# Kernel tuning notes

Hardware: AMD Instinct MI355X
Metric: run time of the kernel (lower is better)

Reference implementation:

```python
import jax, jax.numpy as jnp
import numpy as np

N = 100000
M = 1600000
IN_C = 64
OUT_C = 64


def setup_inputs() -> dict:
    key = jax.random.key(0)
    k1, k2, k3 = jax.random.split(key, 3)
    x = jax.random.normal(k1, (N, IN_C), dtype=jnp.float32)
    edge_index = jax.random.randint(k2, (2, M), 0, N, dtype=jnp.int64)
    # glorot-initialized linear weight (no bias in lin)
    limit = np.sqrt(6.0 / (IN_C + OUT_C))
    W = jax.random.uniform(k3, (IN_C, OUT_C), dtype=jnp.float32, minval=-limit, maxval=limit)
    b = jnp.zeros((OUT_C,), dtype=jnp.float32)  # zeros() init for bias
    return {"x": x, "edge_index": edge_index, "W": W, "b": b}


def reference(x, edge_index, W, b):
    # x: [N, in_c] -> lin -> [N, out_c]
    h = x @ W
    n = x.shape[0]
    row, col = edge_index[0], edge_index[1]  # source, target

    # add self loops (fill_value = 1.0 since improved=False)
    loop = jnp.arange(n, dtype=edge_index.dtype)
    row = jnp.concatenate([row, loop])
    col = jnp.concatenate([col, loop])
    w = jnp.ones(row.shape[0], dtype=h.dtype)  # edge_weight defaults to ones

    # symmetric gcn normalization: deg over target nodes
    deg = jax.ops.segment_sum(w, col, num_segments=n)
    deg_inv_sqrt = deg ** -0.5
    deg_inv_sqrt = jnp.where(jnp.isinf(deg_inv_sqrt), 0.0, deg_inv_sqrt)
    norm = deg_inv_sqrt[row] * w * deg_inv_sqrt[col]  # [M+N]

    # spmm: aggregate normalized source messages at targets
    msgs = norm[:, None] * h[row]  # [M+N, out_c]
    out = jax.ops.segment_sum(msgs, col, num_segments=n)  # [N, out_c]
    return out + b
```

## Files before the change

kernel.cpp:

```cpp
#include <hip/hip_runtime.h>

#define N_NODES 100000
#define M_EDGES 1600000
#define CH 64
#define NPB 256
#define NB ((N_NODES + NPB - 1) / NPB)
#define PART_CHUNK 8192
#define PART_BLOCKS ((M_EDGES + PART_CHUNK - 1) / PART_CHUNK)
#define REG_E 12
#define GROWS 192
#define GBLKS ((N_NODES + GROWS - 1) / GROWS)

__device__ __forceinline__ unsigned int pack_bf16x2(float a, float b) {
    unsigned int ua = __float_as_uint(a);
    ua = (ua + 0x7fffu + ((ua >> 16) & 1u)) >> 16;
    unsigned int ub = __float_as_uint(b);
    ub = (ub + 0x7fffu + ((ub >> 16) & 1u)) >> 16;
    return ua | (ub << 16);
}
__device__ __forceinline__ float bf_lo(unsigned int u) { return __uint_as_float(u << 16); }
__device__ __forceinline__ float bf_hi(unsigned int u) { return __uint_as_float(u & 0xffff0000u); }

__global__ __launch_bounds__(256) void k_bhist(const int* __restrict__ col, int* __restrict__ T) {
    __shared__ int h[NB];
    int tid = threadIdx.x;
    for (int i = tid; i < NB; i += 256) h[i] = 0;
    __syncthreads();
    int start = blockIdx.x * PART_CHUNK;
    int end = min(M_EDGES, start + PART_CHUNK);
    for (int e = start + tid; e < end; e += 256) atomicAdd(&h[col[e] >> 8], 1);
    __syncthreads();
    for (int i = tid; i < NB; i += 256) T[blockIdx.x * NB + i] = h[i];
}

__global__ __launch_bounds__(256) void k_colsum(int* __restrict__ T, int* __restrict__ tot) {
    __shared__ int s[256];
    int b = blockIdx.x, t = threadIdx.x;
    int v = (t < PART_BLOCKS) ? T[t * NB + b] : 0;
    s[t] = v;
    __syncthreads();
    for (int off = 1; off < 256; off <<= 1) {
        int tv = (t >= off) ? s[t - off] : 0;
        __syncthreads();
        s[t] += tv;
        __syncthreads();
    }
    if (t < PART_BLOCKS) T[t * NB + b] = s[t] - v;
    if (t == 255) tot[b] = s[255];
}

__global__ __launch_bounds__(512) void k_bucket_scan(const int* __restrict__ tot, int* __restrict__ bbase) {
    __shared__ int s[512];
    int v = (threadIdx.x < NB) ? tot[threadIdx.x] : 0;
    s[threadIdx.x] = v;
    __syncthreads();
    for (int off = 1; off < 512; off <<= 1) {
        int t = (threadIdx.x >= off) ? s[threadIdx.x - off] : 0;
        __syncthreads();
        s[threadIdx.x] += t;
        __syncthreads();
    }
    if (threadIdx.x < NB) bbase[threadIdx.x] = s[threadIdx.x] - v;
    if (threadIdx.x == NB - 1) bbase[NB] = s[NB - 1];
}

__global__ __launch_bounds__(256) void k_partition(const int* __restrict__ row, const int* __restrict__ col,
                                                   const int* __restrict__ bbase, const int* __restrict__ T,
                                                   unsigned int* __restrict__ pairs) {
    __shared__ int h[NB];
    int tid = threadIdx.x;
    int c = blockIdx.x;
    for (int i = tid; i < NB; i += 256) h[i] = bbase[i] + T[c * NB + i];
    __syncthreads();
    int start = c * PART_CHUNK;
    int end = min(M_EDGES, start + PART_CHUNK);
    for (int e = start + tid; e < end; e += 256) {
        int cc = col[e];
        int pos = atomicAdd(&h[cc >> 8], 1);
        pairs[pos] = ((unsigned int)row[e] << 8) | (unsigned int)(cc & 255);
    }
}

__global__ __launch_bounds__(512) void k_fine(const int* __restrict__ bbase,
                                              unsigned int* __restrict__ pairs, int* __restrict__ node_start,
                                              float* __restrict__ dis) {
    __shared__ int lcnt[NPB];
    __shared__ int lcur[NPB];
    __shared__ int ss[NPB];
    int b = blockIdx.x, t = threadIdx.x;
    int s0 = bbase[b], e0 = bbase[b + 1];

    if (t < NPB) lcnt[t] = 0;
    __syncthreads();

    unsigned int reg[REG_E];
#pragma unroll
    for (int k = 0; k < REG_E; k++) {
        int e = s0 + t + k * 512;
        if (e < e0) {
            unsigned int p = pairs[e];
            reg[k] = p;
            atomicAdd(&lcnt[p & 255u], 1);
        }
    }
    __syncthreads();

    int v = 0;
    if (t < NPB) { v = lcnt[t]; ss[t] = v; }
    __syncthreads();
    for (int off = 1; off < NPB; off <<= 1) {
        int tv = (t < NPB && t >= off) ? ss[t - off] : 0;
        __syncthreads();
        if (t < NPB) ss[t] += tv;
        __syncthreads();
    }
    if (t < NPB) {
        int excl = ss[t] - v;
        lcur[t] = excl;
        int node = b * NPB + t;
        if (node < N_NODES) {
            node_start[node] = s0 + excl;
            dis[node] = 1.0f / sqrtf((float)(v + 1));
        }
        if (b == NB - 1 && t == 0) node_start[N_NODES] = e0;
    }
    __syncthreads();

#pragma unroll
    for (int k = 0; k < REG_E; k++) {
        int e = s0 + t + k * 512;
        if (e < e0) {
            unsigned int p = reg[k];
            int pos = atomicAdd(&lcur[p & 255u], 1);
            pairs[s0 + pos] = p >> 8;
        }
    }
}

__global__ __launch_bounds__(256) void k_gemm_g(const float* __restrict__ x, const float* __restrict__ W,
                                                const float* __restrict__ dis, unsigned int* __restrict__ g2) {
    __shared__ float sW[64][64];
    __shared__ float sXf[GROWS * 65];
    int t = threadIdx.x;
    int row0 = blockIdx.x * GROWS;
    int nrows = min(GROWS, N_NODES - row0);

    for (int i = t; i < 64 * 64; i += 256) sW[i >> 6][i & 63] = W[i];
    const float4* xv = (const float4*)x;
    for (int idx = t; idx < GROWS * 16; idx += 256) {
        int r = idx >> 4, c4 = idx & 15;
        float4 v = (r < nrows) ? xv[(size_t)(row0 + r) * 16 + c4] : make_float4(0.f, 0.f, 0.f, 0.f);
        sXf[r * 65 + c4 * 4 + 0] = v.x;
        sXf[r * 65 + c4 * 4 + 1] = v.y;
        sXf[r * 65 + c4 * 4 + 2] = v.z;
        sXf[r * 65 + c4 * 4 + 3] = v.w;
    }
    __syncthreads();

    int q = t >> 6;
    int rid = t & 63;
    int c0 = q * 16;
    float acc0[16], acc1[16], acc2[16];
#pragma unroll
    for (int j = 0; j < 16; j++) { acc0[j] = 0.f; acc1[j] = 0.f; acc2[j] = 0.f; }

    for (int k = 0; k < 64; k++) {
        float xv0 = sXf[rid * 65 + k];
        float xv1 = sXf[(rid + 64) * 65 + k];
        float xv2 = sXf[(rid + 128) * 65 + k];
        const float4* wp = (const float4*)&sW[k][c0];
        float4 w0 = wp[0], w1 = wp[1], w2 = wp[2], w3 = wp[3];
        float wv[16] = {w0.x, w0.y, w0.z, w0.w, w1.x, w1.y, w1.z, w1.w,
                        w2.x, w2.y, w2.z, w2.w, w3.x, w3.y, w3.z, w3.w};
#pragma unroll
        for (int j = 0; j < 16; j++) {
            acc0[j] += xv0 * wv[j];
            acc1[j] += xv1 * wv[j];
            acc2[j] += xv2 * wv[j];
        }
    }

#pragma unroll
    for (int jr = 0; jr < 3; jr++) {
        int r = rid + jr * 64;
        int gr = row0 + r;
        if (r < nrows) {
            float* accp = (jr == 0) ? acc0 : (jr == 1) ? acc1 : acc2;
            float d = dis[gr];
            uint4 wlo, whi;
            wlo.x = pack_bf16x2(d * accp[0], d * accp[1]);
            wlo.y = pack_bf16x2(d * accp[2], d * accp[3]);
            wlo.z = pack_bf16x2(d * accp[4], d * accp[5]);
            wlo.w = pack_bf16x2(d * accp[6], d * accp[7]);
            whi.x = pack_bf16x2(d * accp[8], d * accp[9]);
            whi.y = pack_bf16x2(d * accp[10], d * accp[11]);
            whi.z = pack_bf16x2(d * accp[12], d * accp[13]);
            whi.w = pack_bf16x2(d * accp[14], d * accp[15]);
            unsigned int base = (unsigned int)gr * 32 + q * 8;
            *reinterpret_cast<uint4*>(&g2[base]) = wlo;
            *reinterpret_cast<uint4*>(&g2[base + 4]) = whi;
        }
    }
}

__global__ __launch_bounds__(256) void k_aggregate(const int* __restrict__ nstart, const int* __restrict__ srow,
                                                   const float* __restrict__ dis, const unsigned int* __restrict__ g2,
                                                   const float* __restrict__ bias, float* __restrict__ out) {
    int node = blockIdx.x * 4 + (threadIdx.x >> 6);
    int l = threadIdx.x & 63;
    if (node >= N_NODES) return;
    int grp = l >> 4;
    int sub = l & 15;
    const uint2* gq = (const uint2*)g2;
    int s0 = nstart[node];
    int e0 = nstart[node + 1];
    float a0 = 0.f, a1 = 0.f, a2 = 0.f, a3 = 0.f;
    int e0m1 = e0 - 1;
    for (int i = s0; i < e0; i += 16) {
        int ea = i + grp, eb = i + 4 + grp, ec = i + 8 + grp, ed = i + 12 + grp;
        int r0 = srow[min(ea, e0m1)];
        int r1 = srow[min(eb, e0m1)];
        int r2 = srow[min(ec, e0m1)];
        int r3 = srow[min(ed, e0m1)];
        uint2 u0 = gq[(unsigned int)r0 * 16 + sub];
        uint2 u1 = gq[(unsigned int)r1 * 16 + sub];
        uint2 u2 = gq[(unsigned int)r2 * 16 + sub];
        uint2 u3 = gq[(unsigned int)r3 * 16 + sub];
        if (ea < e0) { a0 += bf_lo(u0.x); a1 += bf_hi(u0.x); a2 += bf_lo(u0.y); a3 += bf_hi(u0.y); }
        if (eb < e0) { a0 += bf_lo(u1.x); a1 += bf_hi(u1.x); a2 += bf_lo(u1.y); a3 += bf_hi(u1.y); }
        if (ec < e0) { a0 += bf_lo(u2.x); a1 += bf_hi(u2.x); a2 += bf_lo(u2.y); a3 += bf_hi(u2.y); }
        if (ed < e0) { a0 += bf_lo(u3.x); a1 += bf_hi(u3.x); a2 += bf_lo(u3.y); a3 += bf_hi(u3.y); }
    }
    a0 += __shfl_xor(a0, 16, 64); a0 += __shfl_xor(a0, 32, 64);
    a1 += __shfl_xor(a1, 16, 64); a1 += __shfl_xor(a1, 32, 64);
    a2 += __shfl_xor(a2, 16, 64); a2 += __shfl_xor(a2, 32, 64);
    a3 += __shfl_xor(a3, 16, 64); a3 += __shfl_xor(a3, 32, 64);
    if (grp == 0) {
        uint2 su = gq[(unsigned int)node * 16 + sub];
        a0 += bf_lo(su.x); a1 += bf_hi(su.x); a2 += bf_lo(su.y); a3 += bf_hi(su.y);
        float d = dis[node];
        float4 bv = *reinterpret_cast<const float4*>(&bias[4 * sub]);
        float4 o = make_float4(d * a0 + bv.x, d * a1 + bv.y, d * a2 + bv.z, d * a3 + bv.w);
        *reinterpret_cast<float4*>(&out[(size_t)node * CH + 4 * sub]) = o;
    }
}

extern "C" void kernel_launch(void* const* d_in, const int* in_sizes, int n_in,
                              void* d_out, int out_size, void* d_ws, size_t ws_size,
                              hipStream_t stream) {
    const float* x  = (const float*)d_in[0];
    const int*   ei = (const int*)d_in[1];
    const float* W  = (const float*)d_in[2];
    const float* bv = (const float*)d_in[3];
    float* out = (float*)d_out;

    const int* row = ei;
    const int* col = ei + M_EDGES;

    char* ws = (char*)d_ws;
    int*          tot   = (int*)(ws + 0);
    int*          bbase = (int*)(ws + (8 << 10));
    float*        dis   = (float*)(ws + (512 << 10));
    int*          nstart= (int*)(ws + (1024 << 10));
    int*          T     = (int*)(ws + (1536 << 10));
    unsigned int* g2    = (unsigned int*)(ws + (2u << 20));
    unsigned int* pairs = (unsigned int*)(ws + (16u << 20));

    k_bhist<<<PART_BLOCKS, 256, 0, stream>>>(col, T);
    k_colsum<<<NB, 256, 0, stream>>>(T, tot);
    k_bucket_scan<<<1, 512, 0, stream>>>(tot, bbase);
    k_partition<<<PART_BLOCKS, 256, 0, stream>>>(row, col, bbase, T, pairs);
    k_fine<<<NB, 512, 0, stream>>>(bbase, pairs, nstart, dis);
    k_gemm_g<<<GBLKS, 256, 0, stream>>>(x, W, dis, g2);
    k_aggregate<<<(N_NODES + 3) / 4, 256, 0, stream>>>(nstart, (const int*)pairs, dis, g2, bv, out);
}
```

Measured before the change: 209.6 us.

## Halve bucket size, vectorize edge loads, and widen aggregation gathers to 16 bytes

Coarse buckets now cover 128 nodes instead of 256, so the fine sort runs 256-thread blocks with smaller shared histograms, and the bucket scan grows to 1024 threads. The histogram and partition kernels read col and row as int4, cutting load instruction count. Aggregation gives each node 32 lanes, each gathering 16-byte bf16 chunks, which halves the shuffle-reduction width and packs 8 nodes per block. In exchange the partition kernel's per-bucket histogram doubles, per-thread register use for 8 accumulators rises, and workspace offsets are shifted to fit the larger count table.

```diff
diff --git a/kernel.cpp b/kernel.cpp
--- a/kernel.cpp
+++ b/kernel.cpp
@@ -3,7 +3,7 @@
 #define N_NODES 100000
 #define M_EDGES 1600000
 #define CH 64
-#define NPB 256
+#define NPB 128
 #define NB ((N_NODES + NPB - 1) / NPB)
 #define PART_CHUNK 8192
 #define PART_BLOCKS ((M_EDGES + PART_CHUNK - 1) / PART_CHUNK)
@@ -26,9 +26,16 @@
     int tid = threadIdx.x;
     for (int i = tid; i < NB; i += 256) h[i] = 0;
     __syncthreads();
-    int start = blockIdx.x * PART_CHUNK;
-    int end = min(M_EDGES, start + PART_CHUNK);
-    for (int e = start + tid; e < end; e += 256) atomicAdd(&h[col[e] >> 8], 1);
+    const int4* c4 = (const int4*)col;
+    int start4 = blockIdx.x * (PART_CHUNK / 4);
+    int end4 = min(M_EDGES / 4, start4 + PART_CHUNK / 4);
+    for (int e = start4 + tid; e < end4; e += 256) {
+        int4 v = c4[e];
+        atomicAdd(&h[v.x >> 7], 1);
+        atomicAdd(&h[v.y >> 7], 1);
+        atomicAdd(&h[v.z >> 7], 1);
+        atomicAdd(&h[v.w >> 7], 1);
+    }
     __syncthreads();
     for (int i = tid; i < NB; i += 256) T[blockIdx.x * NB + i] = h[i];
 }
@@ -49,19 +56,20 @@
     if (t == 255) tot[b] = s[255];
 }
 
-__global__ __launch_bounds__(512) void k_bucket_scan(const int* __restrict__ tot, int* __restrict__ bbase) {
-    __shared__ int s[512];
-    int v = (threadIdx.x < NB) ? tot[threadIdx.x] : 0;
-    s[threadIdx.x] = v;
-    __syncthreads();
-    for (int off = 1; off < 512; off <<= 1) {
-        int t = (threadIdx.x >= off) ? s[threadIdx.x - off] : 0;
-        __syncthreads();
-        s[threadIdx.x] += t;
-        __syncthreads();
-    }
-    if (threadIdx.x < NB) bbase[threadIdx.x] = s[threadIdx.x] - v;
-    if (threadIdx.x == NB - 1) bbase[NB] = s[NB - 1];
+__global__ __launch_bounds__(1024) void k_bucket_scan(const int* __restrict__ tot, int* __restrict__ bbase) {
+    __shared__ int s[1024];
+    int t = threadIdx.x;
+    int v = (t < NB) ? tot[t] : 0;
+    s[t] = v;
+    __syncthreads();
+    for (int off = 1; off < 1024; off <<= 1) {
+        int tv = (t >= off) ? s[t - off] : 0;
+        __syncthreads();
+        s[t] += tv;
+        __syncthreads();
+    }
+    if (t < NB) bbase[t] = s[t] - v;
+    if (t == NB - 1) bbase[NB] = s[t];
 }
 
 __global__ __launch_bounds__(256) void k_partition(const int* __restrict__ row, const int* __restrict__ col,
@@ -72,16 +80,26 @@
     int c = blockIdx.x;
     for (int i = tid; i < NB; i += 256) h[i] = bbase[i] + T[c * NB + i];
     __syncthreads();
-    int start = c * PART_CHUNK;
-    int end = min(M_EDGES, start + PART_CHUNK);
-    for (int e = start + tid; e < end; e += 256) {
-        int cc = col[e];
-        int pos = atomicAdd(&h[cc >> 8], 1);
-        pairs[pos] = ((unsigned int)row[e] << 8) | (unsigned int)(cc & 255);
-    }
-}
-
-__global__ __launch_bounds__(512) void k_fine(const int* __restrict__ bbase,
+    const int4* c4 = (const int4*)col;
+    const int4* r4 = (const int4*)row;
+    int start4 = c * (PART_CHUNK / 4);
+    int end4 = min(M_EDGES / 4, start4 + PART_CHUNK / 4);
+    for (int e = start4 + tid; e < end4; e += 256) {
+        int4 cc = c4[e];
+        int4 rr = r4[e];
+        int pos;
+        pos = atomicAdd(&h[cc.x >> 7], 1);
+        pairs[pos] = ((unsigned int)rr.x << 7) | (unsigned int)(cc.x & 127);
+        pos = atomicAdd(&h[cc.y >> 7], 1);
+        pairs[pos] = ((unsigned int)rr.y << 7) | (unsigned int)(cc.y & 127);
+        pos = atomicAdd(&h[cc.z >> 7], 1);
+        pairs[pos] = ((unsigned int)rr.z << 7) | (unsigned int)(cc.z & 127);
+        pos = atomicAdd(&h[cc.w >> 7], 1);
+        pairs[pos] = ((unsigned int)rr.w << 7) | (unsigned int)(cc.w & 127);
+    }
+}
+
+__global__ __launch_bounds__(256) void k_fine(const int* __restrict__ bbase,
                                               unsigned int* __restrict__ pairs, int* __restrict__ node_start,
                                               float* __restrict__ dis) {
     __shared__ int lcnt[NPB];
@@ -96,11 +114,11 @@
     unsigned int reg[REG_E];
 #pragma unroll
     for (int k = 0; k < REG_E; k++) {
-        int e = s0 + t + k * 512;
+        int e = s0 + t + k * 256;
         if (e < e0) {
             unsigned int p = pairs[e];
             reg[k] = p;
-            atomicAdd(&lcnt[p & 255u], 1);
+            atomicAdd(&lcnt[p & 127u], 1);
         }
     }
     __syncthreads();
@@ -128,11 +146,11 @@
 
 #pragma unroll
     for (int k = 0; k < REG_E; k++) {
-        int e = s0 + t + k * 512;
+        int e = s0 + t + k * 256;
         if (e < e0) {
             unsigned int p = reg[k];
-            int pos = atomicAdd(&lcur[p & 255u], 1);
-            pairs[s0 + pos] = p >> 8;
+            int pos = atomicAdd(&lcur[p & 127u], 1);
+            pairs[s0 + pos] = p >> 7;
         }
     }
 }
@@ -206,15 +224,15 @@
 __global__ __launch_bounds__(256) void k_aggregate(const int* __restrict__ nstart, const int* __restrict__ srow,
                                                    const float* __restrict__ dis, const unsigned int* __restrict__ g2,
                                                    const float* __restrict__ bias, float* __restrict__ out) {
-    int node = blockIdx.x * 4 + (threadIdx.x >> 6);
-    int l = threadIdx.x & 63;
+    int node = blockIdx.x * 8 + (threadIdx.x >> 5);
     if (node >= N_NODES) return;
-    int grp = l >> 4;
-    int sub = l & 15;
-    const uint2* gq = (const uint2*)g2;
+    int l = threadIdx.x & 31;
+    int grp = l >> 3;
+    int sub = l & 7;
+    const uint4* gq = (const uint4*)g2;
     int s0 = nstart[node];
     int e0 = nstart[node + 1];
-    float a0 = 0.f, a1 = 0.f, a2 = 0.f, a3 = 0.f;
+    float a0 = 0.f, a1 = 0.f, a2 = 0.f, a3 = 0.f, a4 = 0.f, a5 = 0.f, a6 = 0.f, a7 = 0.f;
     int e0m1 = e0 - 1;
     for (int i = s0; i < e0; i += 16) {
         int ea = i + grp, eb = i + 4 + grp, ec = i + 8 + grp, ed = i + 12 + grp;
@@ -222,26 +240,37 @@
         int r1 = srow[min(eb, e0m1)];
         int r2 = srow[min(ec, e0m1)];
         int r3 = srow[min(ed, e0m1)];
-        uint2 u0 = gq[(unsigned int)r0 * 16 + sub];
-        uint2 u1 = gq[(unsigned int)r1 * 16 + sub];
-        uint2 u2 = gq[(unsigned int)r2 * 16 + sub];
-        uint2 u3 = gq[(unsigned int)r3 * 16 + sub];
-        if (ea < e0) { a0 += bf_lo(u0.x); a1 += bf_hi(u0.x); a2 += bf_lo(u0.y); a3 += bf_hi(u0.y); }
-        if (eb < e0) { a0 += bf_lo(u1.x); a1 += bf_hi(u1.x); a2 += bf_lo(u1.y); a3 += bf_hi(u1.y); }
-        if (ec < e0) { a0 += bf_lo(u2.x); a1 += bf_hi(u2.x); a2 += bf_lo(u2.y); a3 += bf_hi(u2.y); }
-        if (ed < e0) { a0 += bf_lo(u3.x); a1 += bf_hi(u3.x); a2 += bf_lo(u3.y); a3 += bf_hi(u3.y); }
-    }
-    a0 += __shfl_xor(a0, 16, 64); a0 += __shfl_xor(a0, 32, 64);
-    a1 += __shfl_xor(a1, 16, 64); a1 += __shfl_xor(a1, 32, 64);
-    a2 += __shfl_xor(a2, 16, 64); a2 += __shfl_xor(a2, 32, 64);
-    a3 += __shfl_xor(a3, 16, 64); a3 += __shfl_xor(a3, 32, 64);
+        uint4 u0 = gq[(unsigned int)r0 * 8 + sub];
+        uint4 u1 = gq[(unsigned int)r1 * 8 + sub];
+        uint4 u2 = gq[(unsigned int)r2 * 8 + sub];
+        uint4 u3 = gq[(unsigned int)r3 * 8 + sub];
+        if (ea < e0) { a0 += bf_lo(u0.x); a1 += bf_hi(u0.x); a2 += bf_lo(u0.y); a3 += bf_hi(u0.y);
+                       a4 += bf_lo(u0.z); a5 += bf_hi(u0.z); a6 += bf_lo(u0.w); a7 += bf_hi(u0.w); }
+        if (eb < e0) { a0 += bf_lo(u1.x); a1 += bf_hi(u1.x); a2 += bf_lo(u1.y); a3 += bf_hi(u1.y);
+                       a4 += bf_lo(u1.z); a5 += bf_hi(u1.z); a6 += bf_lo(u1.w); a7 += bf_hi(u1.w); }
+        if (ec < e0) { a0 += bf_lo(u2.x); a1 += bf_hi(u2.x); a2 += bf_lo(u2.y); a3 += bf_hi(u2.y);
+                       a4 += bf_lo(u2.z); a5 += bf_hi(u2.z); a6 += bf_lo(u2.w); a7 += bf_hi(u2.w); }
+        if (ed < e0) { a0 += bf_lo(u3.x); a1 += bf_hi(u3.x); a2 += bf_lo(u3.y); a3 += bf_hi(u3.y);
+                       a4 += bf_lo(u3.z); a5 += bf_hi(u3.z); a6 += bf_lo(u3.w); a7 += bf_hi(u3.w); }
+    }
+    a0 += __shfl_xor(a0, 8, 64); a0 += __shfl_xor(a0, 16, 64);
+    a1 += __shfl_xor(a1, 8, 64); a1 += __shfl_xor(a1, 16, 64);
+    a2 += __shfl_xor(a2, 8, 64); a2 += __shfl_xor(a2, 16, 64);
+    a3 += __shfl_xor(a3, 8, 64); a3 += __shfl_xor(a3, 16, 64);
+    a4 += __shfl_xor(a4, 8, 64); a4 += __shfl_xor(a4, 16, 64);
+    a5 += __shfl_xor(a5, 8, 64); a5 += __shfl_xor(a5, 16, 64);
+    a6 += __shfl_xor(a6, 8, 64); a6 += __shfl_xor(a6, 16, 64);
+    a7 += __shfl_xor(a7, 8, 64); a7 += __shfl_xor(a7, 16, 64);
     if (grp == 0) {
-        uint2 su = gq[(unsigned int)node * 16 + sub];
+        uint4 su = gq[(unsigned int)node * 8 + sub];
         a0 += bf_lo(su.x); a1 += bf_hi(su.x); a2 += bf_lo(su.y); a3 += bf_hi(su.y);
+        a4 += bf_lo(su.z); a5 += bf_hi(su.z); a6 += bf_lo(su.w); a7 += bf_hi(su.w);
         float d = dis[node];
-        float4 bv = *reinterpret_cast<const float4*>(&bias[4 * sub]);
-        float4 o = make_float4(d * a0 + bv.x, d * a1 + bv.y, d * a2 + bv.z, d * a3 + bv.w);
-        *reinterpret_cast<float4*>(&out[(size_t)node * CH + 4 * sub]) = o;
+        const float4* b4 = (const float4*)bias;
+        float4 bv0 = b4[2 * sub], bv1 = b4[2 * sub + 1];
+        float4* o4 = (float4*)&out[(size_t)node * CH + 8 * sub];
+        o4[0] = make_float4(d * a0 + bv0.x, d * a1 + bv0.y, d * a2 + bv0.z, d * a3 + bv0.w);
+        o4[1] = make_float4(d * a4 + bv1.x, d * a5 + bv1.y, d * a6 + bv1.z, d * a7 + bv1.w);
     }
 }
 
@@ -259,18 +288,18 @@
 
     char* ws = (char*)d_ws;
     int*          tot   = (int*)(ws + 0);
-    int*          bbase = (int*)(ws + (8 << 10));
+    int*          bbase = (int*)(ws + (4 << 10));
     float*        dis   = (float*)(ws + (512 << 10));
     int*          nstart= (int*)(ws + (1024 << 10));
     int*          T     = (int*)(ws + (1536 << 10));
-    unsigned int* g2    = (unsigned int*)(ws + (2u << 20));
+    unsigned int* g2    = (unsigned int*)(ws + (3u << 20));
     unsigned int* pairs = (unsigned int*)(ws + (16u << 20));
 
     k_bhist<<<PART_BLOCKS, 256, 0, stream>>>(col, T);
     k_colsum<<<NB, 256, 0, stream>>>(T, tot);
-    k_bucket_scan<<<1, 512, 0, stream>>>(tot, bbase);
+    k_bucket_scan<<<1, 1024, 0, stream>>>(tot, bbase);
     k_partition<<<PART_BLOCKS, 256, 0, stream>>>(row, col, bbase, T, pairs);
-    k_fine<<<NB, 512, 0, stream>>>(bbase, pairs, nstart, dis);
+    k_fine<<<NB, 256, 0, stream>>>(bbase, pairs, nstart, dis);
     k_gemm_g<<<GBLKS, 256, 0, stream>>>(x, W, dis, g2);
-    k_aggregate<<<(N_NODES + 3) / 4, 256, 0, stream>>>(nstart, (const int*)pairs, dis, g2, bv, out);
-}
+    k_aggregate<<<(N_NODES + 7) / 8, 256, 0, stream>>>(nstart, (const int*)pairs, dis, g2, bv, out);
+}
```

Measured after the change: 184.4 us. 1.14x faster.
